# Kernel optimization log

Hardware: AMD Instinct MI355X
Metric: run time of the kernel (lower is better)

The kernel has to match this reference:

```python
import jax, jax.numpy as jnp
import numpy as np

N_NODES = 50000

def sage_conv(x, src, dst, W_l, b_l, W_r):
    # mean-aggregate neighbor features x[src] at dst, then lin_l(agg)+lin_r(x)
    msgs = x[src]                                       # [E, d]
    agg = jax.ops.segment_sum(msgs, dst, num_segments=N_NODES)
    cnt = jax.ops.segment_sum(jnp.ones((src.shape[0],), x.dtype), dst, num_segments=N_NODES)
    agg = agg / jnp.maximum(cnt, 1.0)[:, None]          # [N, d]
    return agg @ W_l.T + b_l + x @ W_r.T


def setup_inputs() -> dict:
    key = jax.random.key(0)
    ks = jax.random.split(key, 10)
    in_c, hid, out_c = 128, 128, 64
    x = jax.random.normal(ks[0], (N_NODES, in_c), dtype=jnp.float32)
    edge_index = jax.random.randint(ks[1], (2, 800000), 0, N_NODES, dtype=jnp.int64)
    s = 1.0 / np.sqrt(in_c)
    W1_l = jax.random.uniform(ks[2], (hid, in_c), minval=-s, maxval=s)
    b1 = jax.random.uniform(ks[3], (hid,), minval=-s, maxval=s)
    W1_r = jax.random.uniform(ks[4], (hid, in_c), minval=-s, maxval=s)
    s = 1.0 / np.sqrt(hid)
    W2_l = jax.random.uniform(ks[5], (hid, hid), minval=-s, maxval=s)
    b2 = jax.random.uniform(ks[6], (hid,), minval=-s, maxval=s)
    W2_r = jax.random.uniform(ks[7], (hid, hid), minval=-s, maxval=s)
    W3 = jax.random.uniform(ks[8], (out_c, hid), minval=-s, maxval=s)
    b3 = jax.random.uniform(ks[9], (out_c,), minval=-s, maxval=s)
    return {"x": x, "edge_index": edge_index, "W1_l": W1_l, "b1": b1, "W1_r": W1_r,
            "W2_l": W2_l, "b2": b2, "W2_r": W2_r, "W3": W3, "b3": b3}


def reference(x, edge_index, W1_l, b1, W1_r, W2_l, b2, W2_r, W3, b3):
    src, dst = edge_index[0], edge_index[1]
    h = jax.nn.relu(sage_conv(x, src, dst, W1_l, b1, W1_r))
    h = jax.nn.relu(sage_conv(h, src, dst, W2_l, b2, W2_r))
    return h @ W3.T + b3
```

## Files before the change

kernel.cpp:

```cpp
#include <hip/hip_runtime.h>

#define FDIM 128

typedef __attribute__((ext_vector_type(8))) short bf16x8;
typedef __attribute__((ext_vector_type(4))) float f32x4;

static __device__ __forceinline__ ushort f2bf(float f) {
    uint u = __float_as_uint(f);
    uint r = (u + 0x7FFF + ((u >> 16) & 1)) >> 16;
    return (ushort)r;
}
static __device__ __forceinline__ uint packbf(float lo, float hi) {
    return (uint)f2bf(lo) | ((uint)f2bf(hi) << 16);
}
static __device__ __forceinline__ float bflo(uint v) { return __uint_as_float(v << 16); }
static __device__ __forceinline__ float bfhi(uint v) { return __uint_as_float(v & 0xFFFF0000u); }


__global__ void prep_kernel(const float* __restrict__ x, ushort* __restrict__ xb, int nx8,
                            const float* __restrict__ W1l, const float* __restrict__ W1r,
                            const float* __restrict__ W2l, const float* __restrict__ W2r,
                            const float* __restrict__ W3, ushort* __restrict__ wbuf,
                            const int* __restrict__ dst, int E, int* __restrict__ bcnt,
                            int nconv) {
    const int b = blockIdx.x;
    const int tid = threadIdx.x;
    if (b < nconv) {
        int i = b * 256 + tid;
        if (i < nx8) {
            const float* s = x + (size_t)i * 8;
            float4 a = *(const float4*)(s);
            float4 c = *(const float4*)(s + 4);
            uint4 o;
            o.x = packbf(a.x, a.y); o.y = packbf(a.z, a.w);
            o.z = packbf(c.x, c.y); o.w = packbf(c.z, c.w);
            *(uint4*)(xb + (size_t)i * 8) = o;
        }
    } else if (b < nconv + 36) {
        int c = (b - nconv) * 256 + tid;
        const float* s; ushort* d;
        if (c < 2048)      { s = W1l + (size_t)c * 8;          d = wbuf + (size_t)c * 8; }
        else if (c < 4096) { s = W1r + (size_t)(c - 2048) * 8; d = wbuf + 16384 + (size_t)(c - 2048) * 8; }
        else if (c < 6144) { s = W2l + (size_t)(c - 4096) * 8; d = wbuf + 32768 + (size_t)(c - 4096) * 8; }
        else if (c < 8192) { s = W2r + (size_t)(c - 6144) * 8; d = wbuf + 49152 + (size_t)(c - 6144) * 8; }
        else               { s = W3  + (size_t)(c - 8192) * 8; d = wbuf + 65536 + (size_t)(c - 8192) * 8; }
        float4 a = *(const float4*)(s);
        float4 cc = *(const float4*)(s + 4);
        uint4 o;
        o.x = packbf(a.x, a.y); o.y = packbf(a.z, a.w);
        o.z = packbf(cc.x, cc.y); o.w = packbf(cc.z, cc.w);
        *(uint4*)d = o;
    } else {
        __shared__ int lh[256];
        int hb = b - nconv - 36;
        lh[tid] = 0;
        __syncthreads();
        #pragma unroll
        for (int k = 0; k < 8; ++k) {
            int e = hb * 2048 + k * 256 + tid;
            if (e < E) atomicAdd(&lh[dst[e] >> 8], 1);
        }
        __syncthreads();
        if (lh[tid]) atomicAdd(&bcnt[tid], lh[tid]);
    }
}


__global__ void scan_buckets(const int* __restrict__ bcnt, int* __restrict__ bbase,
                             int* __restrict__ bcur, int nb) {
    const int lane = threadIdx.x;
    const int i0 = lane * 4;
    int v0 = (i0 + 0 < nb) ? bcnt[i0 + 0] : 0;
    int v1 = (i0 + 1 < nb) ? bcnt[i0 + 1] : 0;
    int v2 = (i0 + 2 < nb) ? bcnt[i0 + 2] : 0;
    int v3 = (i0 + 3 < nb) ? bcnt[i0 + 3] : 0;
    int s = v0 + v1 + v2 + v3;
    int incl = s;
    #pragma unroll
    for (int d = 1; d < 64; d <<= 1) {
        int t = __shfl_up(incl, d);
        if (lane >= d) incl += t;
    }
    int excl = incl - s;
    int e0 = excl, e1 = excl + v0, e2 = e1 + v1, e3 = e2 + v2;
    if (i0 + 0 < nb) { bbase[i0 + 0] = e0; bcur[i0 + 0] = e0; }
    if (i0 + 1 < nb) { bbase[i0 + 1] = e1; bcur[i0 + 1] = e1; }
    if (i0 + 2 < nb) { bbase[i0 + 2] = e2; bcur[i0 + 2] = e2; }
    if (i0 + 3 < nb) { bbase[i0 + 3] = e3; bcur[i0 + 3] = e3; }
    int total = __shfl(incl, 63);
    if (lane == 0) bbase[nb] = total;
}


__global__ void pair_scatter(const int* __restrict__ src, const int* __restrict__ dst,
                             int* __restrict__ bcur, uint* __restrict__ pairs, int E) {
    __shared__ int lh[256];
    __shared__ int gb[256];
    const int tid = threadIdx.x;
    lh[tid] = 0;
    __syncthreads();
    int ss[8], dd[8], sl[8];
    #pragma unroll
    for (int k = 0; k < 8; ++k) {
        int e = blockIdx.x * 2048 + k * 256 + tid;
        if (e < E) {
            ss[k] = src[e];
            dd[k] = dst[e];
            sl[k] = atomicAdd(&lh[dd[k] >> 8], 1);
        } else dd[k] = -1;
    }
    __syncthreads();
    if (lh[tid]) gb[tid] = atomicAdd(&bcur[tid], lh[tid]);
    __syncthreads();
    #pragma unroll
    for (int k = 0; k < 8; ++k) {
        if (dd[k] >= 0)
            pairs[gb[dd[k] >> 8] + sl[k]] = (uint)ss[k] | ((uint)(dd[k] & 255) << 24);
    }
}


__global__ void bucket_csr(const uint* __restrict__ pairs, const int* __restrict__ bbase,
                           int* __restrict__ off, int* __restrict__ csr, int N) {
    __shared__ int cnt[256];
    __shared__ int base[256];
    __shared__ int cur[256];
    const int b = blockIdx.x;
    const int tid = threadIdx.x;
    const int p0 = bbase[b], p1 = bbase[b + 1];
    cnt[tid] = 0;
    __syncthreads();
    for (int p = p0 + tid; p < p1; p += 256) atomicAdd(&cnt[pairs[p] >> 24], 1);
    __syncthreads();
    if (tid < 64) {
        int i0 = tid * 4;
        int v0 = cnt[i0], v1 = cnt[i0 + 1], v2 = cnt[i0 + 2], v3 = cnt[i0 + 3];
        int s = v0 + v1 + v2 + v3;
        int incl = s;
        #pragma unroll
        for (int d = 1; d < 64; d <<= 1) {
            int t = __shfl_up(incl, d);
            if (tid >= d) incl += t;
        }
        int excl = incl - s;
        base[i0] = excl; base[i0 + 1] = excl + v0;
        base[i0 + 2] = excl + v0 + v1; base[i0 + 3] = excl + v0 + v1 + v2;
        cur[i0] = base[i0]; cur[i0 + 1] = base[i0 + 1];
        cur[i0 + 2] = base[i0 + 2]; cur[i0 + 3] = base[i0 + 3];
    }
    __syncthreads();
    int node = (b << 8) + tid;
    if (node <= N) off[node] = p0 + base[tid];
    for (int p = p0 + tid; p < p1; p += 256) {
        uint e = pairs[p];
        int slot = atomicAdd(&cur[e >> 24], 1);
        csr[p0 + slot] = (int)(e & 0xFFFFFF);
    }
}


__global__ void agg_kernel(const ushort* __restrict__ feat, const int* __restrict__ off,
                           const int* __restrict__ csr, ushort* __restrict__ agg, int n) {
    int node = blockIdx.x * 4 + (threadIdx.x >> 6);
    if (node >= n) return;
    const int lane = threadIdx.x & 63;
    const int g = lane >> 4;
    const int c = lane & 15;
    const int j0 = off[node], j1 = off[node + 1];
    float a[8] = {0.f, 0.f, 0.f, 0.f, 0.f, 0.f, 0.f, 0.f};
    int j = j0 + g;
    for (; j + 12 < j1; j += 16) {
        int s0 = csr[j], s1 = csr[j + 4], s2 = csr[j + 8], s3 = csr[j + 12];
        uint4 v0 = *(const uint4*)(feat + (size_t)s0 * FDIM + c * 8);
        uint4 v1 = *(const uint4*)(feat + (size_t)s1 * FDIM + c * 8);
        uint4 v2 = *(const uint4*)(feat + (size_t)s2 * FDIM + c * 8);
        uint4 v3 = *(const uint4*)(feat + (size_t)s3 * FDIM + c * 8);
        a[0] += bflo(v0.x) + bflo(v1.x) + bflo(v2.x) + bflo(v3.x);
        a[1] += bfhi(v0.x) + bfhi(v1.x) + bfhi(v2.x) + bfhi(v3.x);
        a[2] += bflo(v0.y) + bflo(v1.y) + bflo(v2.y) + bflo(v3.y);
        a[3] += bfhi(v0.y) + bfhi(v1.y) + bfhi(v2.y) + bfhi(v3.y);
        a[4] += bflo(v0.z) + bflo(v1.z) + bflo(v2.z) + bflo(v3.z);
        a[5] += bfhi(v0.z) + bfhi(v1.z) + bfhi(v2.z) + bfhi(v3.z);
        a[6] += bflo(v0.w) + bflo(v1.w) + bflo(v2.w) + bflo(v3.w);
        a[7] += bfhi(v0.w) + bfhi(v1.w) + bfhi(v2.w) + bfhi(v3.w);
    }
    for (; j + 4 < j1; j += 8) {
        int s0 = csr[j], s1 = csr[j + 4];
        uint4 v0 = *(const uint4*)(feat + (size_t)s0 * FDIM + c * 8);
        uint4 v1 = *(const uint4*)(feat + (size_t)s1 * FDIM + c * 8);
        a[0] += bflo(v0.x) + bflo(v1.x); a[1] += bfhi(v0.x) + bfhi(v1.x);
        a[2] += bflo(v0.y) + bflo(v1.y); a[3] += bfhi(v0.y) + bfhi(v1.y);
        a[4] += bflo(v0.z) + bflo(v1.z); a[5] += bfhi(v0.z) + bfhi(v1.z);
        a[6] += bflo(v0.w) + bflo(v1.w); a[7] += bfhi(v0.w) + bfhi(v1.w);
    }
    for (; j < j1; j += 4) {
        int s0 = csr[j];
        uint4 v0 = *(const uint4*)(feat + (size_t)s0 * FDIM + c * 8);
        a[0] += bflo(v0.x); a[1] += bfhi(v0.x);
        a[2] += bflo(v0.y); a[3] += bfhi(v0.y);
        a[4] += bflo(v0.z); a[5] += bfhi(v0.z);
        a[6] += bflo(v0.w); a[7] += bfhi(v0.w);
    }
    #pragma unroll
    for (int k = 0; k < 8; ++k) {
        a[k] += __shfl_xor(a[k], 16);
        a[k] += __shfl_xor(a[k], 32);
    }
    if (g == 0) {
        float inv = 1.0f / fmaxf((float)(j1 - j0), 1.0f);
        uint4 o;
        o.x = packbf(a[0] * inv, a[1] * inv);
        o.y = packbf(a[2] * inv, a[3] * inv);
        o.z = packbf(a[4] * inv, a[5] * inv);
        o.w = packbf(a[6] * inv, a[7] * inv);
        *(uint4*)(agg + (size_t)node * FDIM + c * 8) = o;
    }
}


template<int RELU>
__global__ void sage_linear_mfma(const ushort* __restrict__ agg, const ushort* __restrict__ xin,
                                 const ushort* __restrict__ Wl, const ushort* __restrict__ Wr,
                                 const float* __restrict__ bias, ushort* __restrict__ out, int n) {
    __shared__ __align__(16) ushort As[32 * FDIM];
    __shared__ __align__(16) ushort Xs[32 * FDIM];
    const int row0 = blockIdx.x * 32;
    const int lane = threadIdx.x & 63;
    const int wid  = threadIdx.x >> 6;
    const int wrow = wid & 1;
    const int wcol = wid >> 1;

    const float4 z4 = make_float4(0.f, 0.f, 0.f, 0.f);
    #pragma unroll
    for (int i = 0; i < 2; ++i) {
        int s = threadIdx.x + i * 256;
        int r = s >> 4, cch = s & 15;
        int row = row0 + r;
        float4 va = z4, vx = z4;
        if (row < n) {
            va = *(const float4*)(agg + (size_t)row * FDIM + cch * 8);
            vx = *(const float4*)(xin + (size_t)row * FDIM + cch * 8);
        }
        int sc = cch ^ (r & 7);
        *(float4*)(As + (r * 16 + sc) * 8) = va;
        *(float4*)(Xs + (r * 16 + sc) * 8) = vx;
    }
    __syncthreads();

    const int lr = lane & 15;
    const int lk = lane >> 4;

    f32x4 acc[4];
    #pragma unroll
    for (int t = 0; t < 4; ++t) acc[t] = (f32x4){0.f, 0.f, 0.f, 0.f};

    const int arow = wrow * 16 + lr;
    #pragma unroll
    for (int ks = 0; ks < 4; ++ks) {
        bf16x8 a = *(const bf16x8*)(As + (arow * 16 + ((ks * 4 + lk) ^ (arow & 7))) * 8);
        #pragma unroll
        for (int t = 0; t < 4; ++t) {
            int wr = wcol * 64 + t * 16 + lr;
            bf16x8 bb = *(const bf16x8*)(Wl + (size_t)wr * FDIM + ks * 32 + lk * 8);
            acc[t] = __builtin_amdgcn_mfma_f32_16x16x32_bf16(a, bb, acc[t], 0, 0, 0);
        }
    }
    #pragma unroll
    for (int ks = 0; ks < 4; ++ks) {
        bf16x8 a = *(const bf16x8*)(Xs + (arow * 16 + ((ks * 4 + lk) ^ (arow & 7))) * 8);
        #pragma unroll
        for (int t = 0; t < 4; ++t) {
            int wr = wcol * 64 + t * 16 + lr;
            bf16x8 bb = *(const bf16x8*)(Wr + (size_t)wr * FDIM + ks * 32 + lk * 8);
            acc[t] = __builtin_amdgcn_mfma_f32_16x16x32_bf16(a, bb, acc[t], 0, 0, 0);
        }
    }

    #pragma unroll
    for (int t = 0; t < 4; ++t) {
        int col = wcol * 64 + t * 16 + lr;
        float bc = bias[col];
        #pragma unroll
        for (int j = 0; j < 4; ++j) {
            int row = row0 + wrow * 16 + lk * 4 + j;
            if (row < n) {
                float v = acc[t][j] + bc;
                if (RELU) v = fmaxf(v, 0.f);
                out[(size_t)row * FDIM + col] = f2bf(v);
            }
        }
    }
}


__global__ void sage_linear2_head(const ushort* __restrict__ agg, const ushort* __restrict__ xin,
                                  const ushort* __restrict__ Wl, const ushort* __restrict__ Wr,
                                  const float* __restrict__ bias,
                                  const ushort* __restrict__ W3, const float* __restrict__ b3,
                                  float* __restrict__ out, int n) {
    __shared__ __align__(16) ushort As[32 * FDIM];
    __shared__ __align__(16) ushort Xs[32 * FDIM];
    const int row0 = blockIdx.x * 32;
    const int lane = threadIdx.x & 63;
    const int wid  = threadIdx.x >> 6;
    const int wrow = wid & 1;
    const int wcol = wid >> 1;

    const float4 z4 = make_float4(0.f, 0.f, 0.f, 0.f);
    #pragma unroll
    for (int i = 0; i < 2; ++i) {
        int s = threadIdx.x + i * 256;
        int r = s >> 4, cch = s & 15;
        int row = row0 + r;
        float4 va = z4, vx = z4;
        if (row < n) {
            va = *(const float4*)(agg + (size_t)row * FDIM + cch * 8);
            vx = *(const float4*)(xin + (size_t)row * FDIM + cch * 8);
        }
        int sc = cch ^ (r & 7);
        *(float4*)(As + (r * 16 + sc) * 8) = va;
        *(float4*)(Xs + (r * 16 + sc) * 8) = vx;
    }
    __syncthreads();

    const int lr = lane & 15;
    const int lk = lane >> 4;

    f32x4 acc[4];
    #pragma unroll
    for (int t = 0; t < 4; ++t) acc[t] = (f32x4){0.f, 0.f, 0.f, 0.f};

    const int arow = wrow * 16 + lr;
    #pragma unroll
    for (int ks = 0; ks < 4; ++ks) {
        bf16x8 a = *(const bf16x8*)(As + (arow * 16 + ((ks * 4 + lk) ^ (arow & 7))) * 8);
        #pragma unroll
        for (int t = 0; t < 4; ++t) {
            int wr = wcol * 64 + t * 16 + lr;
            bf16x8 bb = *(const bf16x8*)(Wl + (size_t)wr * FDIM + ks * 32 + lk * 8);
            acc[t] = __builtin_amdgcn_mfma_f32_16x16x32_bf16(a, bb, acc[t], 0, 0, 0);
        }
    }
    #pragma unroll
    for (int ks = 0; ks < 4; ++ks) {
        bf16x8 a = *(const bf16x8*)(Xs + (arow * 16 + ((ks * 4 + lk) ^ (arow & 7))) * 8);
        #pragma unroll
        for (int t = 0; t < 4; ++t) {
            int wr = wcol * 64 + t * 16 + lr;
            bf16x8 bb = *(const bf16x8*)(Wr + (size_t)wr * FDIM + ks * 32 + lk * 8);
            acc[t] = __builtin_amdgcn_mfma_f32_16x16x32_bf16(a, bb, acc[t], 0, 0, 0);
        }
    }

    __syncthreads();
    #pragma unroll
    for (int t = 0; t < 4; ++t) {
        int col = wcol * 64 + t * 16 + lr;
        float bc = bias[col];
        #pragma unroll
        for (int j = 0; j < 4; ++j) {
            int r = wrow * 16 + lk * 4 + j;
            float v = fmaxf(acc[t][j] + bc, 0.f);
            As[(r * 16 + ((col >> 3) ^ (r & 7))) * 8 + (col & 7)] = f2bf(v);
        }
    }
    __syncthreads();

    f32x4 acc2[2];
    #pragma unroll
    for (int t = 0; t < 2; ++t) acc2[t] = (f32x4){0.f, 0.f, 0.f, 0.f};

    #pragma unroll
    for (int ks = 0; ks < 4; ++ks) {
        bf16x8 a = *(const bf16x8*)(As + (arow * 16 + ((ks * 4 + lk) ^ (arow & 7))) * 8);
        #pragma unroll
        for (int t = 0; t < 2; ++t) {
            int wr = wcol * 32 + t * 16 + lr;
            bf16x8 bb = *(const bf16x8*)(W3 + (size_t)wr * FDIM + ks * 32 + lk * 8);
            acc2[t] = __builtin_amdgcn_mfma_f32_16x16x32_bf16(a, bb, acc2[t], 0, 0, 0);
        }
    }

    #pragma unroll
    for (int t = 0; t < 2; ++t) {
        int col = wcol * 32 + t * 16 + lr;
        float bc = b3[col];
        #pragma unroll
        for (int j = 0; j < 4; ++j) {
            int row = row0 + wrow * 16 + lk * 4 + j;
            if (row < n) out[(size_t)row * 64 + col] = acc2[t][j] + bc;
        }
    }
}


extern "C" void kernel_launch(void* const* d_in, const int* in_sizes, int n_in,
                              void* d_out, int out_size, void* d_ws, size_t ws_size,
                              hipStream_t stream) {
    const float* x   = (const float*)d_in[0];
    const int*   ei  = (const int*)d_in[1];
    const float* W1l = (const float*)d_in[2];
    const float* b1  = (const float*)d_in[3];
    const float* W1r = (const float*)d_in[4];
    const float* W2l = (const float*)d_in[5];
    const float* b2  = (const float*)d_in[6];
    const float* W2r = (const float*)d_in[7];
    const float* W3  = (const float*)d_in[8];
    const float* b3  = (const float*)d_in[9];
    float* out = (float*)d_out;

    const int N = in_sizes[0] / FDIM;
    const int E = in_sizes[1] / 2;
    const int* src = ei;
    const int* dst = ei + E;
    const int NBK = (N + 255) >> 8;

    char* ws = (char*)d_ws;
    size_t p = 0;
    auto alloc = [&](size_t bytes) {
        char* q = ws + p;
        p += (bytes + 255) & ~(size_t)255;
        return q;
    };
    int* bcnt    = (int*)alloc(256 * 4);
    int* bbase   = (int*)alloc(260 * 4);
    int* bcur    = (int*)alloc(256 * 4);
    uint* pairs  = (uint*)alloc((size_t)E * 4);
    int* csr     = (int*)alloc((size_t)E * 4);
    int* off     = (int*)alloc((size_t)(N + 1) * 4);
    ushort* xb   = (ushort*)alloc((size_t)N * FDIM * 2);
    ushort* agb  = (ushort*)alloc((size_t)N * FDIM * 2);
    ushort* h1b  = (ushort*)alloc((size_t)N * FDIM * 2);
    ushort* wbuf = (ushort*)alloc(73728 * 2);
    ushort* w1l = wbuf, *w1r = wbuf + 16384, *w2l = wbuf + 32768,
           *w2r = wbuf + 49152, *w3 = wbuf + 65536;

    hipMemsetAsync(bcnt, 0, 256 * 4, stream);

    const int nx8   = N * FDIM / 8;
    const int nconv = (nx8 + 255) / 256;
    const int nhist = (E + 2047) / 2048;
    prep_kernel<<<nconv + 36 + nhist, 256, 0, stream>>>(
        x, xb, nx8, W1l, W1r, W2l, W2r, W3, wbuf, dst, E, bcnt, nconv);
    scan_buckets<<<1, 64, 0, stream>>>(bcnt, bbase, bcur, NBK);
    pair_scatter<<<(E + 2047) / 2048, 256, 0, stream>>>(src, dst, bcur, pairs, E);
    bucket_csr<<<NBK, 256, 0, stream>>>(pairs, bbase, off, csr, N);

    const int lgrid = (N + 31) / 32;
    agg_kernel<<<(N + 3) / 4, 256, 0, stream>>>(xb, off, csr, agb, N);
    sage_linear_mfma<1><<<lgrid, 256, 0, stream>>>(agb, xb, w1l, w1r, b1, h1b, N);
    agg_kernel<<<(N + 3) / 4, 256, 0, stream>>>(h1b, off, csr, agb, N);
    sage_linear2_head<<<lgrid, 256, 0, stream>>>(agb, h1b, w2l, w2r, b2, w3, b3, out, N);
}
```

Baseline: 181.3 us.

## Fuse neighbor mean-aggregation into SAGE linear MFMA kernels

```diff
diff --git a/kernel.cpp b/kernel.cpp
--- a/kernel.cpp
+++ b/kernel.cpp
@@ -159,76 +159,18 @@
 }
 
 
-__global__ void agg_kernel(const ushort* __restrict__ feat, const int* __restrict__ off,
-                           const int* __restrict__ csr, ushort* __restrict__ agg, int n) {
-    int node = blockIdx.x * 4 + (threadIdx.x >> 6);
-    if (node >= n) return;
-    const int lane = threadIdx.x & 63;
-    const int g = lane >> 4;
-    const int c = lane & 15;
-    const int j0 = off[node], j1 = off[node + 1];
-    float a[8] = {0.f, 0.f, 0.f, 0.f, 0.f, 0.f, 0.f, 0.f};
-    int j = j0 + g;
-    for (; j + 12 < j1; j += 16) {
-        int s0 = csr[j], s1 = csr[j + 4], s2 = csr[j + 8], s3 = csr[j + 12];
-        uint4 v0 = *(const uint4*)(feat + (size_t)s0 * FDIM + c * 8);
-        uint4 v1 = *(const uint4*)(feat + (size_t)s1 * FDIM + c * 8);
-        uint4 v2 = *(const uint4*)(feat + (size_t)s2 * FDIM + c * 8);
-        uint4 v3 = *(const uint4*)(feat + (size_t)s3 * FDIM + c * 8);
-        a[0] += bflo(v0.x) + bflo(v1.x) + bflo(v2.x) + bflo(v3.x);
-        a[1] += bfhi(v0.x) + bfhi(v1.x) + bfhi(v2.x) + bfhi(v3.x);
-        a[2] += bflo(v0.y) + bflo(v1.y) + bflo(v2.y) + bflo(v3.y);
-        a[3] += bfhi(v0.y) + bfhi(v1.y) + bfhi(v2.y) + bfhi(v3.y);
-        a[4] += bflo(v0.z) + bflo(v1.z) + bflo(v2.z) + bflo(v3.z);
-        a[5] += bfhi(v0.z) + bfhi(v1.z) + bfhi(v2.z) + bfhi(v3.z);
-        a[6] += bflo(v0.w) + bflo(v1.w) + bflo(v2.w) + bflo(v3.w);
-        a[7] += bfhi(v0.w) + bfhi(v1.w) + bfhi(v2.w) + bfhi(v3.w);
-    }
-    for (; j + 4 < j1; j += 8) {
-        int s0 = csr[j], s1 = csr[j + 4];
-        uint4 v0 = *(const uint4*)(feat + (size_t)s0 * FDIM + c * 8);
-        uint4 v1 = *(const uint4*)(feat + (size_t)s1 * FDIM + c * 8);
-        a[0] += bflo(v0.x) + bflo(v1.x); a[1] += bfhi(v0.x) + bfhi(v1.x);
-        a[2] += bflo(v0.y) + bflo(v1.y); a[3] += bfhi(v0.y) + bfhi(v1.y);
-        a[4] += bflo(v0.z) + bflo(v1.z); a[5] += bfhi(v0.z) + bfhi(v1.z);
-        a[6] += bflo(v0.w) + bflo(v1.w); a[7] += bfhi(v0.w) + bfhi(v1.w);
-    }
-    for (; j < j1; j += 4) {
-        int s0 = csr[j];
-        uint4 v0 = *(const uint4*)(feat + (size_t)s0 * FDIM + c * 8);
-        a[0] += bflo(v0.x); a[1] += bfhi(v0.x);
-        a[2] += bflo(v0.y); a[3] += bfhi(v0.y);
-        a[4] += bflo(v0.z); a[5] += bfhi(v0.z);
-        a[6] += bflo(v0.w); a[7] += bfhi(v0.w);
-    }
-    #pragma unroll
-    for (int k = 0; k < 8; ++k) {
-        a[k] += __shfl_xor(a[k], 16);
-        a[k] += __shfl_xor(a[k], 32);
-    }
-    if (g == 0) {
-        float inv = 1.0f / fmaxf((float)(j1 - j0), 1.0f);
-        uint4 o;
-        o.x = packbf(a[0] * inv, a[1] * inv);
-        o.y = packbf(a[2] * inv, a[3] * inv);
-        o.z = packbf(a[4] * inv, a[5] * inv);
-        o.w = packbf(a[6] * inv, a[7] * inv);
-        *(uint4*)(agg + (size_t)node * FDIM + c * 8) = o;
-    }
-}
-
-
-template<int RELU>
-__global__ void sage_linear_mfma(const ushort* __restrict__ agg, const ushort* __restrict__ xin,
-                                 const ushort* __restrict__ Wl, const ushort* __restrict__ Wr,
-                                 const float* __restrict__ bias, ushort* __restrict__ out, int n) {
+template<int HEAD>
+__global__ void fused_sage(const ushort* __restrict__ feat, const int* __restrict__ off,
+                           const int* __restrict__ csr,
+                           const ushort* __restrict__ Wl, const ushort* __restrict__ Wr,
+                           const float* __restrict__ bias,
+                           const ushort* __restrict__ W3, const float* __restrict__ b3,
+                           ushort* __restrict__ hout, float* __restrict__ fout, int n) {
     __shared__ __align__(16) ushort As[32 * FDIM];
     __shared__ __align__(16) ushort Xs[32 * FDIM];
     const int row0 = blockIdx.x * 32;
     const int lane = threadIdx.x & 63;
     const int wid  = threadIdx.x >> 6;
-    const int wrow = wid & 1;
-    const int wcol = wid >> 1;
 
     const float4 z4 = make_float4(0.f, 0.f, 0.f, 0.f);
     #pragma unroll
@@ -236,17 +178,72 @@
         int s = threadIdx.x + i * 256;
         int r = s >> 4, cch = s & 15;
         int row = row0 + r;
-        float4 va = z4, vx = z4;
-        if (row < n) {
-            va = *(const float4*)(agg + (size_t)row * FDIM + cch * 8);
-            vx = *(const float4*)(xin + (size_t)row * FDIM + cch * 8);
-        }
-        int sc = cch ^ (r & 7);
-        *(float4*)(As + (r * 16 + sc) * 8) = va;
-        *(float4*)(Xs + (r * 16 + sc) * 8) = vx;
-    }
-    __syncthreads();
-
+        float4 vx = (row < n) ? *(const float4*)(feat + (size_t)row * FDIM + cch * 8) : z4;
+        *(float4*)(Xs + (r * 16 + (cch ^ (r & 7))) * 8) = vx;
+    }
+
+    const int g = lane >> 4;
+    const int c = lane & 15;
+    for (int i = 0; i < 8; ++i) {
+        const int r = wid * 8 + i;
+        const int node = row0 + r;
+        float a[8] = {0.f, 0.f, 0.f, 0.f, 0.f, 0.f, 0.f, 0.f};
+        float inv = 0.f;
+        if (node < n) {
+            const int j0 = off[node], j1 = off[node + 1];
+            int j = j0 + g;
+            for (; j + 12 < j1; j += 16) {
+                int s0 = csr[j], s1 = csr[j + 4], s2 = csr[j + 8], s3 = csr[j + 12];
+                uint4 v0 = *(const uint4*)(feat + (size_t)s0 * FDIM + c * 8);
+                uint4 v1 = *(const uint4*)(feat + (size_t)s1 * FDIM + c * 8);
+                uint4 v2 = *(const uint4*)(feat + (size_t)s2 * FDIM + c * 8);
+                uint4 v3 = *(const uint4*)(feat + (size_t)s3 * FDIM + c * 8);
+                a[0] += bflo(v0.x) + bflo(v1.x) + bflo(v2.x) + bflo(v3.x);
+                a[1] += bfhi(v0.x) + bfhi(v1.x) + bfhi(v2.x) + bfhi(v3.x);
+                a[2] += bflo(v0.y) + bflo(v1.y) + bflo(v2.y) + bflo(v3.y);
+                a[3] += bfhi(v0.y) + bfhi(v1.y) + bfhi(v2.y) + bfhi(v3.y);
+                a[4] += bflo(v0.z) + bflo(v1.z) + bflo(v2.z) + bflo(v3.z);
+                a[5] += bfhi(v0.z) + bfhi(v1.z) + bfhi(v2.z) + bfhi(v3.z);
+                a[6] += bflo(v0.w) + bflo(v1.w) + bflo(v2.w) + bflo(v3.w);
+                a[7] += bfhi(v0.w) + bfhi(v1.w) + bfhi(v2.w) + bfhi(v3.w);
+            }
+            for (; j + 4 < j1; j += 8) {
+                int s0 = csr[j], s1 = csr[j + 4];
+                uint4 v0 = *(const uint4*)(feat + (size_t)s0 * FDIM + c * 8);
+                uint4 v1 = *(const uint4*)(feat + (size_t)s1 * FDIM + c * 8);
+                a[0] += bflo(v0.x) + bflo(v1.x); a[1] += bfhi(v0.x) + bfhi(v1.x);
+                a[2] += bflo(v0.y) + bflo(v1.y); a[3] += bfhi(v0.y) + bfhi(v1.y);
+                a[4] += bflo(v0.z) + bflo(v1.z); a[5] += bfhi(v0.z) + bfhi(v1.z);
+                a[6] += bflo(v0.w) + bflo(v1.w); a[7] += bfhi(v0.w) + bfhi(v1.w);
+            }
+            for (; j < j1; j += 4) {
+                int s0 = csr[j];
+                uint4 v0 = *(const uint4*)(feat + (size_t)s0 * FDIM + c * 8);
+                a[0] += bflo(v0.x); a[1] += bfhi(v0.x);
+                a[2] += bflo(v0.y); a[3] += bfhi(v0.y);
+                a[4] += bflo(v0.z); a[5] += bfhi(v0.z);
+                a[6] += bflo(v0.w); a[7] += bfhi(v0.w);
+            }
+            inv = 1.0f / fmaxf((float)(j1 - j0), 1.0f);
+        }
+        #pragma unroll
+        for (int k = 0; k < 8; ++k) {
+            a[k] += __shfl_xor(a[k], 16);
+            a[k] += __shfl_xor(a[k], 32);
+        }
+        if (g == 0) {
+            uint4 o;
+            o.x = packbf(a[0] * inv, a[1] * inv);
+            o.y = packbf(a[2] * inv, a[3] * inv);
+            o.z = packbf(a[4] * inv, a[5] * inv);
+            o.w = packbf(a[6] * inv, a[7] * inv);
+            *(uint4*)(As + (r * 16 + (c ^ (r & 7))) * 8) = o;
+        }
+    }
+    __syncthreads();
+
+    const int wrow = wid & 1;
+    const int wcol = wid >> 1;
     const int lr = lane & 15;
     const int lk = lane >> 4;
 
@@ -276,119 +273,59 @@
         }
     }
 
-    #pragma unroll
-    for (int t = 0; t < 4; ++t) {
-        int col = wcol * 64 + t * 16 + lr;
-        float bc = bias[col];
-        #pragma unroll
-        for (int j = 0; j < 4; ++j) {
-            int row = row0 + wrow * 16 + lk * 4 + j;
-            if (row < n) {
-                float v = acc[t][j] + bc;
-                if (RELU) v = fmaxf(v, 0.f);
-                out[(size_t)row * FDIM + col] = f2bf(v);
-            }
-        }
-    }
-}
-
-
-__global__ void sage_linear2_head(const ushort* __restrict__ agg, const ushort* __restrict__ xin,
-                                  const ushort* __restrict__ Wl, const ushort* __restrict__ Wr,
-                                  const float* __restrict__ bias,
-                                  const ushort* __restrict__ W3, const float* __restrict__ b3,
-                                  float* __restrict__ out, int n) {
-    __shared__ __align__(16) ushort As[32 * FDIM];
-    __shared__ __align__(16) ushort Xs[32 * FDIM];
-    const int row0 = blockIdx.x * 32;
-    const int lane = threadIdx.x & 63;
-    const int wid  = threadIdx.x >> 6;
-    const int wrow = wid & 1;
-    const int wcol = wid >> 1;
-
-    const float4 z4 = make_float4(0.f, 0.f, 0.f, 0.f);
-    #pragma unroll
-    for (int i = 0; i < 2; ++i) {
-        int s = threadIdx.x + i * 256;
-        int r = s >> 4, cch = s & 15;
-        int row = row0 + r;
-        float4 va = z4, vx = z4;
-        if (row < n) {
-            va = *(const float4*)(agg + (size_t)row * FDIM + cch * 8);
-            vx = *(const float4*)(xin + (size_t)row * FDIM + cch * 8);
-        }
-        int sc = cch ^ (r & 7);
-        *(float4*)(As + (r * 16 + sc) * 8) = va;
-        *(float4*)(Xs + (r * 16 + sc) * 8) = vx;
-    }
-    __syncthreads();
-
-    const int lr = lane & 15;
-    const int lk = lane >> 4;
-
-    f32x4 acc[4];
-    #pragma unroll
-    for (int t = 0; t < 4; ++t) acc[t] = (f32x4){0.f, 0.f, 0.f, 0.f};
-
-    const int arow = wrow * 16 + lr;
-    #pragma unroll
-    for (int ks = 0; ks < 4; ++ks) {
-        bf16x8 a = *(const bf16x8*)(As + (arow * 16 + ((ks * 4 + lk) ^ (arow & 7))) * 8);
+    if (HEAD == 0) {
         #pragma unroll
         for (int t = 0; t < 4; ++t) {
-            int wr = wcol * 64 + t * 16 + lr;
-            bf16x8 bb = *(const bf16x8*)(Wl + (size_t)wr * FDIM + ks * 32 + lk * 8);
-            acc[t] = __builtin_amdgcn_mfma_f32_16x16x32_bf16(a, bb, acc[t], 0, 0, 0);
-        }
-    }
-    #pragma unroll
-    for (int ks = 0; ks < 4; ++ks) {
-        bf16x8 a = *(const bf16x8*)(Xs + (arow * 16 + ((ks * 4 + lk) ^ (arow & 7))) * 8);
+            int col = wcol * 64 + t * 16 + lr;
+            float bc = bias[col];
+            #pragma unroll
+            for (int j = 0; j < 4; ++j) {
+                int row = row0 + wrow * 16 + lk * 4 + j;
+                if (row < n) {
+                    float v = fmaxf(acc[t][j] + bc, 0.f);
+                    hout[(size_t)row * FDIM + col] = f2bf(v);
+                }
+            }
+        }
+    } else {
+        __syncthreads();
         #pragma unroll
         for (int t = 0; t < 4; ++t) {
-            int wr = wcol * 64 + t * 16 + lr;
-            bf16x8 bb = *(const bf16x8*)(Wr + (size_t)wr * FDIM + ks * 32 + lk * 8);
-            acc[t] = __builtin_amdgcn_mfma_f32_16x16x32_bf16(a, bb, acc[t], 0, 0, 0);
-        }
-    }
-
-    __syncthreads();
-    #pragma unroll
-    for (int t = 0; t < 4; ++t) {
-        int col = wcol * 64 + t * 16 + lr;
-        float bc = bias[col];
-        #pragma unroll
-        for (int j = 0; j < 4; ++j) {
-            int r = wrow * 16 + lk * 4 + j;
-            float v = fmaxf(acc[t][j] + bc, 0.f);
-            As[(r * 16 + ((col >> 3) ^ (r & 7))) * 8 + (col & 7)] = f2bf(v);
-        }
-    }
-    __syncthreads();
-
-    f32x4 acc2[2];
-    #pragma unroll
-    for (int t = 0; t < 2; ++t) acc2[t] = (f32x4){0.f, 0.f, 0.f, 0.f};
-
-    #pragma unroll
-    for (int ks = 0; ks < 4; ++ks) {
-        bf16x8 a = *(const bf16x8*)(As + (arow * 16 + ((ks * 4 + lk) ^ (arow & 7))) * 8);
+            int col = wcol * 64 + t * 16 + lr;
+            float bc = bias[col];
+            #pragma unroll
+            for (int j = 0; j < 4; ++j) {
+                int r = wrow * 16 + lk * 4 + j;
+                float v = fmaxf(acc[t][j] + bc, 0.f);
+                As[(r * 16 + ((col >> 3) ^ (r & 7))) * 8 + (col & 7)] = f2bf(v);
+            }
+        }
+        __syncthreads();
+
+        f32x4 acc2[2];
+        #pragma unroll
+        for (int t = 0; t < 2; ++t) acc2[t] = (f32x4){0.f, 0.f, 0.f, 0.f};
+
+        #pragma unroll
+        for (int ks = 0; ks < 4; ++ks) {
+            bf16x8 a = *(const bf16x8*)(As + (arow * 16 + ((ks * 4 + lk) ^ (arow & 7))) * 8);
+            #pragma unroll
+            for (int t = 0; t < 2; ++t) {
+                int wr = wcol * 32 + t * 16 + lr;
+                bf16x8 bb = *(const bf16x8*)(W3 + (size_t)wr * FDIM + ks * 32 + lk * 8);
+                acc2[t] = __builtin_amdgcn_mfma_f32_16x16x32_bf16(a, bb, acc2[t], 0, 0, 0);
+            }
+        }
+
         #pragma unroll
         for (int t = 0; t < 2; ++t) {
-            int wr = wcol * 32 + t * 16 + lr;
-            bf16x8 bb = *(const bf16x8*)(W3 + (size_t)wr * FDIM + ks * 32 + lk * 8);
-            acc2[t] = __builtin_amdgcn_mfma_f32_16x16x32_bf16(a, bb, acc2[t], 0, 0, 0);
-        }
-    }
-
-    #pragma unroll
-    for (int t = 0; t < 2; ++t) {
-        int col = wcol * 32 + t * 16 + lr;
-        float bc = b3[col];
-        #pragma unroll
-        for (int j = 0; j < 4; ++j) {
-            int row = row0 + wrow * 16 + lk * 4 + j;
-            if (row < n) out[(size_t)row * 64 + col] = acc2[t][j] + bc;
+            int col = wcol * 32 + t * 16 + lr;
+            float bc = b3[col];
+            #pragma unroll
+            for (int j = 0; j < 4; ++j) {
+                int row = row0 + wrow * 16 + lk * 4 + j;
+                if (row < n) fout[(size_t)row * 64 + col] = acc2[t][j] + bc;
+            }
         }
     }
 }
@@ -429,7 +366,6 @@
     int* csr     = (int*)alloc((size_t)E * 4);
     int* off     = (int*)alloc((size_t)(N + 1) * 4);
     ushort* xb   = (ushort*)alloc((size_t)N * FDIM * 2);
-    ushort* agb  = (ushort*)alloc((size_t)N * FDIM * 2);
     ushort* h1b  = (ushort*)alloc((size_t)N * FDIM * 2);
     ushort* wbuf = (ushort*)alloc(73728 * 2);
     ushort* w1l = wbuf, *w1r = wbuf + 16384, *w2l = wbuf + 32768,
@@ -447,8 +383,9 @@
     bucket_csr<<<NBK, 256, 0, stream>>>(pairs, bbase, off, csr, N);
 
     const int lgrid = (N + 31) / 32;
-    agg_kernel<<<(N + 3) / 4, 256, 0, stream>>>(xb, off, csr, agb, N);
-    sage_linear_mfma<1><<<lgrid, 256, 0, stream>>>(agb, xb, w1l, w1r, b1, h1b, N);
-    agg_kernel<<<(N + 3) / 4, 256, 0, stream>>>(h1b, off, csr, agb, N);
-    sage_linear2_head<<<lgrid, 256, 0, stream>>>(agb, h1b, w2l, w2r, b2, w3, b3, out, N);
-}
+    fused_sage<0><<<lgrid, 256, 0, stream>>>(xb, off, csr, w1l, w1r, b1,
+                                             (const ushort*)nullptr, (const float*)nullptr,
+                                             h1b, (float*)nullptr, N);
+    fused_sage<1><<<lgrid, 256, 0, stream>>>(h1b, off, csr, w2l, w2r, b2,
+                                             w3, b3, (ushort*)nullptr, out, N);
+}
```

New measurement: 169.7 us. 1.07x faster.

## Split features into 32-column slabs for cache-resident gather; fuse bucket scan into histogram

Applied to the files above, without the earlier changes.

```diff
diff --git a/kernel.cpp b/kernel.cpp
--- a/kernel.cpp
+++ b/kernel.cpp
@@ -17,12 +17,14 @@
 static __device__ __forceinline__ float bfhi(uint v) { return __uint_as_float(v & 0xFFFF0000u); }
 
 
-__global__ void prep_kernel(const float* __restrict__ x, ushort* __restrict__ xb, int nx8,
+__global__ void prep_kernel(const float* __restrict__ x, ushort* __restrict__ xbn,
+                            ushort* __restrict__ xbs, int nx8, int slabElems,
                             const float* __restrict__ W1l, const float* __restrict__ W1r,
                             const float* __restrict__ W2l, const float* __restrict__ W2r,
                             const float* __restrict__ W3, ushort* __restrict__ wbuf,
                             const int* __restrict__ dst, int E, int* __restrict__ bcnt,
-                            int nconv) {
+                            int* __restrict__ hdone, int* __restrict__ bbase,
+                            int* __restrict__ bcur, int nb, int nconv, int nhist) {
     const int b = blockIdx.x;
     const int tid = threadIdx.x;
     if (b < nconv) {
@@ -34,7 +36,9 @@
             uint4 o;
             o.x = packbf(a.x, a.y); o.y = packbf(a.z, a.w);
             o.z = packbf(c.x, c.y); o.w = packbf(c.z, c.w);
-            *(uint4*)(xb + (size_t)i * 8) = o;
+            *(uint4*)(xbn + (size_t)i * 8) = o;
+            int node = i >> 4, cch = i & 15;
+            *(uint4*)(xbs + (size_t)(cch >> 2) * slabElems + (size_t)node * 32 + (cch & 3) * 8) = o;
         }
     } else if (b < nconv + 36) {
         int c = (b - nconv) * 256 + tid;
@@ -52,6 +56,7 @@
         *(uint4*)d = o;
     } else {
         __shared__ int lh[256];
+        __shared__ int isLast;
         int hb = b - nconv - 36;
         lh[tid] = 0;
         __syncthreads();
@@ -62,33 +67,37 @@
         }
         __syncthreads();
         if (lh[tid]) atomicAdd(&bcnt[tid], lh[tid]);
-    }
-}
-
-
-__global__ void scan_buckets(const int* __restrict__ bcnt, int* __restrict__ bbase,
-                             int* __restrict__ bcur, int nb) {
-    const int lane = threadIdx.x;
-    const int i0 = lane * 4;
-    int v0 = (i0 + 0 < nb) ? bcnt[i0 + 0] : 0;
-    int v1 = (i0 + 1 < nb) ? bcnt[i0 + 1] : 0;
-    int v2 = (i0 + 2 < nb) ? bcnt[i0 + 2] : 0;
-    int v3 = (i0 + 3 < nb) ? bcnt[i0 + 3] : 0;
-    int s = v0 + v1 + v2 + v3;
-    int incl = s;
-    #pragma unroll
-    for (int d = 1; d < 64; d <<= 1) {
-        int t = __shfl_up(incl, d);
-        if (lane >= d) incl += t;
-    }
-    int excl = incl - s;
-    int e0 = excl, e1 = excl + v0, e2 = e1 + v1, e3 = e2 + v2;
-    if (i0 + 0 < nb) { bbase[i0 + 0] = e0; bcur[i0 + 0] = e0; }
-    if (i0 + 1 < nb) { bbase[i0 + 1] = e1; bcur[i0 + 1] = e1; }
-    if (i0 + 2 < nb) { bbase[i0 + 2] = e2; bcur[i0 + 2] = e2; }
-    if (i0 + 3 < nb) { bbase[i0 + 3] = e3; bcur[i0 + 3] = e3; }
-    int total = __shfl(incl, 63);
-    if (lane == 0) bbase[nb] = total;
+        __syncthreads();
+        if (tid == 0) {
+            __threadfence();
+            isLast = (atomicAdd(hdone, 1) == nhist - 1);
+        }
+        __syncthreads();
+        if (isLast && tid < 64) {
+            __threadfence();
+            volatile int* vb = bcnt;
+            const int i0 = tid * 4;
+            int v0 = (i0 + 0 < nb) ? vb[i0 + 0] : 0;
+            int v1 = (i0 + 1 < nb) ? vb[i0 + 1] : 0;
+            int v2 = (i0 + 2 < nb) ? vb[i0 + 2] : 0;
+            int v3 = (i0 + 3 < nb) ? vb[i0 + 3] : 0;
+            int s = v0 + v1 + v2 + v3;
+            int incl = s;
+            #pragma unroll
+            for (int d = 1; d < 64; d <<= 1) {
+                int t = __shfl_up(incl, d);
+                if (tid >= d) incl += t;
+            }
+            int excl = incl - s;
+            int e0 = excl, e1 = excl + v0, e2 = e1 + v1, e3 = e2 + v2;
+            if (i0 + 0 < nb) { bbase[i0 + 0] = e0; bcur[i0 + 0] = e0; }
+            if (i0 + 1 < nb) { bbase[i0 + 1] = e1; bcur[i0 + 1] = e1; }
+            if (i0 + 2 < nb) { bbase[i0 + 2] = e2; bcur[i0 + 2] = e2; }
+            if (i0 + 3 < nb) { bbase[i0 + 3] = e3; bcur[i0 + 3] = e3; }
+            int total = __shfl(incl, 63);
+            if (tid == 0) bbase[nb] = total;
+        }
+    }
 }
 
 
@@ -159,69 +168,52 @@
 }
 
 
-__global__ void agg_kernel(const ushort* __restrict__ feat, const int* __restrict__ off,
-                           const int* __restrict__ csr, ushort* __restrict__ agg, int n) {
-    int node = blockIdx.x * 4 + (threadIdx.x >> 6);
-    if (node >= n) return;
+__global__ __launch_bounds__(256, 8)
+void agg_slice(const ushort* __restrict__ slab, const int* __restrict__ off,
+               const int* __restrict__ csr, ushort* __restrict__ agg, int p, int n) {
     const int lane = threadIdx.x & 63;
-    const int g = lane >> 4;
-    const int c = lane & 15;
-    const int j0 = off[node], j1 = off[node + 1];
-    float a[8] = {0.f, 0.f, 0.f, 0.f, 0.f, 0.f, 0.f, 0.f};
-    int j = j0 + g;
-    for (; j + 12 < j1; j += 16) {
-        int s0 = csr[j], s1 = csr[j + 4], s2 = csr[j + 8], s3 = csr[j + 12];
-        uint4 v0 = *(const uint4*)(feat + (size_t)s0 * FDIM + c * 8);
-        uint4 v1 = *(const uint4*)(feat + (size_t)s1 * FDIM + c * 8);
-        uint4 v2 = *(const uint4*)(feat + (size_t)s2 * FDIM + c * 8);
-        uint4 v3 = *(const uint4*)(feat + (size_t)s3 * FDIM + c * 8);
-        a[0] += bflo(v0.x) + bflo(v1.x) + bflo(v2.x) + bflo(v3.x);
-        a[1] += bfhi(v0.x) + bfhi(v1.x) + bfhi(v2.x) + bfhi(v3.x);
-        a[2] += bflo(v0.y) + bflo(v1.y) + bflo(v2.y) + bflo(v3.y);
-        a[3] += bfhi(v0.y) + bfhi(v1.y) + bfhi(v2.y) + bfhi(v3.y);
-        a[4] += bflo(v0.z) + bflo(v1.z) + bflo(v2.z) + bflo(v3.z);
-        a[5] += bfhi(v0.z) + bfhi(v1.z) + bfhi(v2.z) + bfhi(v3.z);
-        a[6] += bflo(v0.w) + bflo(v1.w) + bflo(v2.w) + bflo(v3.w);
-        a[7] += bfhi(v0.w) + bfhi(v1.w) + bfhi(v2.w) + bfhi(v3.w);
-    }
-    for (; j + 4 < j1; j += 8) {
-        int s0 = csr[j], s1 = csr[j + 4];
-        uint4 v0 = *(const uint4*)(feat + (size_t)s0 * FDIM + c * 8);
-        uint4 v1 = *(const uint4*)(feat + (size_t)s1 * FDIM + c * 8);
-        a[0] += bflo(v0.x) + bflo(v1.x); a[1] += bfhi(v0.x) + bfhi(v1.x);
-        a[2] += bflo(v0.y) + bflo(v1.y); a[3] += bfhi(v0.y) + bfhi(v1.y);
-        a[4] += bflo(v0.z) + bflo(v1.z); a[5] += bfhi(v0.z) + bfhi(v1.z);
-        a[6] += bflo(v0.w) + bflo(v1.w); a[7] += bfhi(v0.w) + bfhi(v1.w);
-    }
-    for (; j < j1; j += 4) {
-        int s0 = csr[j];
-        uint4 v0 = *(const uint4*)(feat + (size_t)s0 * FDIM + c * 8);
-        a[0] += bflo(v0.x); a[1] += bfhi(v0.x);
-        a[2] += bflo(v0.y); a[3] += bfhi(v0.y);
-        a[4] += bflo(v0.z); a[5] += bfhi(v0.z);
-        a[6] += bflo(v0.w); a[7] += bfhi(v0.w);
-    }
-    #pragma unroll
-    for (int k = 0; k < 8; ++k) {
-        a[k] += __shfl_xor(a[k], 16);
-        a[k] += __shfl_xor(a[k], 32);
-    }
-    if (g == 0) {
-        float inv = 1.0f / fmaxf((float)(j1 - j0), 1.0f);
-        uint4 o;
-        o.x = packbf(a[0] * inv, a[1] * inv);
-        o.y = packbf(a[2] * inv, a[3] * inv);
-        o.z = packbf(a[4] * inv, a[5] * inv);
-        o.w = packbf(a[6] * inv, a[7] * inv);
-        *(uint4*)(agg + (size_t)node * FDIM + c * 8) = o;
-    }
-}
-
-
-template<int RELU>
+    const int wid  = threadIdx.x >> 6;
+    const int g = lane >> 3;
+    const int q = lane & 7;
+    for (int i = 0; i < 4; ++i) {
+        const int node = blockIdx.x * 16 + wid * 4 + i;
+        if (node >= n) return;
+        const int j0 = off[node], j1 = off[node + 1];
+        float a0 = 0.f, a1 = 0.f, a2 = 0.f, a3 = 0.f;
+        int j = j0 + g;
+        for (; j + 8 < j1; j += 16) {
+            int s0 = csr[j], s1 = csr[j + 8];
+            uint2 v0 = *(const uint2*)(slab + (size_t)s0 * 32 + q * 4);
+            uint2 v1 = *(const uint2*)(slab + (size_t)s1 * 32 + q * 4);
+            a0 += bflo(v0.x) + bflo(v1.x); a1 += bfhi(v0.x) + bfhi(v1.x);
+            a2 += bflo(v0.y) + bflo(v1.y); a3 += bfhi(v0.y) + bfhi(v1.y);
+        }
+        if (j < j1) {
+            uint2 v0 = *(const uint2*)(slab + (size_t)csr[j] * 32 + q * 4);
+            a0 += bflo(v0.x); a1 += bfhi(v0.x);
+            a2 += bflo(v0.y); a3 += bfhi(v0.y);
+        }
+        a0 += __shfl_xor(a0, 8);  a1 += __shfl_xor(a1, 8);
+        a2 += __shfl_xor(a2, 8);  a3 += __shfl_xor(a3, 8);
+        a0 += __shfl_xor(a0, 16); a1 += __shfl_xor(a1, 16);
+        a2 += __shfl_xor(a2, 16); a3 += __shfl_xor(a3, 16);
+        a0 += __shfl_xor(a0, 32); a1 += __shfl_xor(a1, 32);
+        a2 += __shfl_xor(a2, 32); a3 += __shfl_xor(a3, 32);
+        if (g == 0) {
+            float inv = 1.0f / fmaxf((float)(j1 - j0), 1.0f);
+            uint2 o;
+            o.x = packbf(a0 * inv, a1 * inv);
+            o.y = packbf(a2 * inv, a3 * inv);
+            *(uint2*)(agg + (size_t)node * FDIM + p * 32 + q * 4) = o;
+        }
+    }
+}
+
+
 __global__ void sage_linear_mfma(const ushort* __restrict__ agg, const ushort* __restrict__ xin,
                                  const ushort* __restrict__ Wl, const ushort* __restrict__ Wr,
-                                 const float* __restrict__ bias, ushort* __restrict__ out, int n) {
+                                 const float* __restrict__ bias, ushort* __restrict__ outn,
+                                 ushort* __restrict__ outs, int slabElems, int n) {
     __shared__ __align__(16) ushort As[32 * FDIM];
     __shared__ __align__(16) ushort Xs[32 * FDIM];
     const int row0 = blockIdx.x * 32;
@@ -280,13 +272,14 @@
     for (int t = 0; t < 4; ++t) {
         int col = wcol * 64 + t * 16 + lr;
         float bc = bias[col];
+        ushort* slb = outs + (size_t)(col >> 5) * slabElems + (col & 31);
         #pragma unroll
         for (int j = 0; j < 4; ++j) {
             int row = row0 + wrow * 16 + lk * 4 + j;
             if (row < n) {
-                float v = acc[t][j] + bc;
-                if (RELU) v = fmaxf(v, 0.f);
-                out[(size_t)row * FDIM + col] = f2bf(v);
+                ushort hv = f2bf(fmaxf(acc[t][j] + bc, 0.f));
+                outn[(size_t)row * FDIM + col] = hv;
+                slb[(size_t)row * 32] = hv;
             }
         }
     }
@@ -414,6 +407,7 @@
     const int* src = ei;
     const int* dst = ei + E;
     const int NBK = (N + 255) >> 8;
+    const int slabElems = N * 32;
 
     char* ws = (char*)d_ws;
     size_t p = 0;
@@ -422,33 +416,42 @@
         p += (bytes + 255) & ~(size_t)255;
         return q;
     };
-    int* bcnt    = (int*)alloc(256 * 4);
+    int* ctrl    = (int*)alloc(272 * 4);
+    int* bcnt    = ctrl;
+    int* hdone   = ctrl + 256;
     int* bbase   = (int*)alloc(260 * 4);
     int* bcur    = (int*)alloc(256 * 4);
     uint* pairs  = (uint*)alloc((size_t)E * 4);
     int* csr     = (int*)alloc((size_t)E * 4);
     int* off     = (int*)alloc((size_t)(N + 1) * 4);
-    ushort* xb   = (ushort*)alloc((size_t)N * FDIM * 2);
+    ushort* xbn  = (ushort*)alloc((size_t)N * FDIM * 2);
+    ushort* xbs  = (ushort*)alloc((size_t)N * FDIM * 2);
+    ushort* h1n  = (ushort*)alloc((size_t)N * FDIM * 2);
+    ushort* h1s  = (ushort*)alloc((size_t)N * FDIM * 2);
     ushort* agb  = (ushort*)alloc((size_t)N * FDIM * 2);
-    ushort* h1b  = (ushort*)alloc((size_t)N * FDIM * 2);
     ushort* wbuf = (ushort*)alloc(73728 * 2);
     ushort* w1l = wbuf, *w1r = wbuf + 16384, *w2l = wbuf + 32768,
            *w2r = wbuf + 49152, *w3 = wbuf + 65536;
 
-    hipMemsetAsync(bcnt, 0, 256 * 4, stream);
+    hipMemsetAsync(ctrl, 0, 257 * 4, stream);
 
     const int nx8   = N * FDIM / 8;
     const int nconv = (nx8 + 255) / 256;
     const int nhist = (E + 2047) / 2048;
     prep_kernel<<<nconv + 36 + nhist, 256, 0, stream>>>(
-        x, xb, nx8, W1l, W1r, W2l, W2r, W3, wbuf, dst, E, bcnt, nconv);
-    scan_buckets<<<1, 64, 0, stream>>>(bcnt, bbase, bcur, NBK);
+        x, xbn, xbs, nx8, slabElems, W1l, W1r, W2l, W2r, W3, wbuf, dst, E, bcnt,
+        hdone, bbase, bcur, NBK, nconv, nhist);
     pair_scatter<<<(E + 2047) / 2048, 256, 0, stream>>>(src, dst, bcur, pairs, E);
     bucket_csr<<<NBK, 256, 0, stream>>>(pairs, bbase, off, csr, N);
 
+    const int ggrid = (N + 15) / 16;
     const int lgrid = (N + 31) / 32;
-    agg_kernel<<<(N + 3) / 4, 256, 0, stream>>>(xb, off, csr, agb, N);
-    sage_linear_mfma<1><<<lgrid, 256, 0, stream>>>(agb, xb, w1l, w1r, b1, h1b, N);
-    agg_kernel<<<(N + 3) / 4, 256, 0, stream>>>(h1b, off, csr, agb, N);
-    sage_linear2_head<<<lgrid, 256, 0, stream>>>(agb, h1b, w2l, w2r, b2, w3, b3, out, N);
-}
+
+    for (int s = 0; s < 4; ++s)
+        agg_slice<<<ggrid, 256, 0, stream>>>(xbs + (size_t)s * slabElems, off, csr, agb, s, N);
+    sage_linear_mfma<<<lgrid, 256, 0, stream>>>(agb, xbn, w1l, w1r, b1, h1n, h1s, slabElems, N);
+
+    for (int s = 0; s < 4; ++s)
+        agg_slice<<<ggrid, 256, 0, stream>>>(h1s + (size_t)s * slabElems, off, csr, agb, s, N);
+    sage_linear2_head<<<lgrid, 256, 0, stream>>>(agb, h1n, w2l, w2r, b2, w3, b3, out, N);
+}
```

Measured after the change: 274.4 us. 1.51x slower.
